# Kernel tuning notes

Hardware: AMD Instinct MI355X
Metric: run time of the kernel (lower is better)

Reference implementation:

```python
import jax, jax.numpy as jnp
import numpy as np

DIM = 256   # model dim (forced by gate Linear(32,4): d = 32 = DIM//H)
H = 8       # heads (hard-coded by mask.repeat(1,8,1,1))
D = DIM // H
B = 256     # batch
NS = 100    # skeleton tokens (sub-block size)
NQ = 64     # query tokens
N = NS + NQ # 164
NE = 4      # experts
HID = 50    # expert hidden
LN_EPS = 1e-5


def setup_inputs() -> dict:
    key = jax.random.key(0)
    ks = jax.random.split(key, 12)
    s = 0.02
    return {
        "x": jax.random.normal(ks[0], (B, N, DIM), jnp.float32),
        "mask": jax.random.randint(ks[1], (B, N), 0, 2).astype(bool),
        "w_qk_s": jax.random.normal(ks[2], (DIM, 2 * DIM), jnp.float32) * s,
        "w_qk_q": jax.random.normal(ks[3], (DIM, 2 * DIM), jnp.float32) * s,
        "w_v": jax.random.normal(ks[4], (DIM, DIM), jnp.float32) * s,
        "w_gate": jax.random.normal(ks[5], (D, NE), jnp.float32) * s,
        "b_gate": jnp.zeros((NE,), jnp.float32),
        "ln_gamma": jnp.ones((NE,), jnp.float32),
        "ln_beta": jnp.zeros((NE,), jnp.float32),
        "w1": jax.random.normal(ks[6], (NE, NS, HID), jnp.float32) * s,
        "b1": jnp.zeros((NE, HID), jnp.float32),
        "w2": jax.random.normal(ks[7], (NE, HID, NS), jnp.float32) * s,
        "b2": jnp.zeros((NE, NS), jnp.float32),
        "w_out": jax.random.normal(ks[8], (DIM, DIM), jnp.float32) * s,
        "b_out": jnp.zeros((DIM,), jnp.float32),
    }


def reference(x, mask, w_qk_s, w_qk_q, w_v, w_gate, b_gate, ln_gamma, ln_beta,
              w1, b1, w2, b2, w_out, b_out):
    b, n, dim = x.shape
    scale = dim ** -0.5  # scale_with_head=False -> dim**-0.5

    def to_heads(t):  # (b, m, H*D) -> (b, H, m, D)
        return t.reshape(b, -1, H, D).transpose(0, 2, 1, 3)

    # separate qk projections for skeleton (first 100) vs query (last 64) tokens
    q_s, k_s = jnp.split(x[:, :NS] @ w_qk_s, 2, axis=-1)
    q_q, k_q = jnp.split(x[:, NS:] @ w_qk_q, 2, axis=-1)
    q = jnp.concatenate([to_heads(q_s), to_heads(q_q)], axis=2)  # (b,H,N,D)
    k = jnp.concatenate([to_heads(k_s), to_heads(k_q)], axis=2)
    v = to_heads(x @ w_v)

    # gates: RAW reshape of x (b,n,H*D) -> (b,H,n,D) (memory reinterpretation,
    # as in torch x.reshape), detached, sliced to first 100 'rows'
    gx = jax.lax.stop_gradient(x).reshape(b, H, n, D)[:, :, :NS, :]
    g = gx @ w_gate + b_gate                              # (b,H,100,4)
    mu = g.mean(-1, keepdims=True)
    var = g.var(-1, keepdims=True)
    g = (g - mu) / jnp.sqrt(var + LN_EPS) * ln_gamma + ln_beta
    gates = jax.nn.softmax(g, axis=-1)                    # (b,H,100,4)

    dots = jnp.einsum('bhid,bhjd->bhij', q, k) * scale    # (b,H,N,N)
    mask_value = -jnp.finfo(dots.dtype).max
    dots = jnp.where(mask[:, None, None, :], mask_value, dots)

    # soft-MoE over the 100x100 sub-block (experts applied along key axis)
    attn_q = dots[:, :, :NS, :NS]                         # (b,H,100,100)
    h1 = jax.nn.relu(jnp.einsum('bhij,ejk->bheik', jax.nn.relu(attn_q), w1)
                     + b1[:, None, :])                    # (b,H,4,100,50)
    eo = jax.nn.relu(jnp.einsum('bheik,ekj->bheij', h1, w2)
                     + b2[:, None, :])                    # (b,H,4,100,100)
    moes = jnp.einsum('bheij,bhie->bhij', eo, gates)      # (b,H,100,100)

    dots = dots.at[:, :, :NS, :NS].add(moes)
    attn = jax.nn.softmax(dots, axis=-1)
    out = jnp.einsum('bhij,bhjd->bhid', attn, v)          # (b,H,N,D)
    out = out.transpose(0, 2, 1, 3).reshape(b, n, dim)
    return out @ w_out + b_out
```

## Files before the change

kernel.cpp:

```cpp
#include <hip/hip_runtime.h>

typedef __bf16 bf16x8 __attribute__((ext_vector_type(8)));
typedef __bf16 bf16x4 __attribute__((ext_vector_type(4)));
typedef float  f32x4  __attribute__((ext_vector_type(4)));

__device__ __forceinline__ bf16x8 ldb8(const __bf16* p) {
    return *reinterpret_cast<const bf16x8*>(p);
}
__device__ __forceinline__ bf16x8 zero8() {
    bf16x8 z;
    #pragma unroll
    for (int i = 0; i < 8; i++) z[i] = (__bf16)0.f;
    return z;
}
__device__ __forceinline__ __bf16 ldw(const void* p, int i, int m) {
    return m ? (__bf16)((const float*)p)[i] : ((const __bf16*)p)[i];
}
__device__ __forceinline__ bf16x8 ldx8(const void* p, size_t ei, int m) {
    if (m) {
        const float* f = (const float*)p + ei;
        f32x4 a = *reinterpret_cast<const f32x4*>(f);
        f32x4 b = *reinterpret_cast<const f32x4*>(f + 4);
        bf16x8 r;
        #pragma unroll
        for (int u = 0; u < 4; u++) { r[u] = (__bf16)a[u]; r[4 + u] = (__bf16)b[u]; }
        return r;
    }
    return ldb8((const __bf16*)p + ei);
}

__global__ __launch_bounds__(256) void detect_kernel(
    const void* x, const void* mask, int* modes, int* maskws)
{
    __shared__ int v32bad, v16bad, sbad;
    const int t = threadIdx.x, bid = blockIdx.x;
    if (t == 0) { v32bad = 0; v16bad = 0; sbad = 0; }
    __syncthreads();
    const unsigned int* mw = (const unsigned int*)mask;
    int b32 = 0, b16 = 0;
    for (int i = t; i < 10496; i += 256) {
        unsigned int w = mw[i];
        if (!(w == 0u || w == 1u || w == 0x3F800000u)) b32++;
        unsigned int h0 = w & 0xFFFFu, h1 = w >> 16;
        if (!(h0 == 0u || h0 == 1u || h0 == 0x3F80u)) b16++;
        if (!(h1 == 0u || h1 == 1u || h1 == 0x3F80u)) b16++;
    }
    if (b32) atomicAdd(&v32bad, b32);
    if (b16) atomicAdd(&v16bad, b16);
    if (bid == 0) {
        const unsigned int* xw = (const unsigned int*)x;
        int bad = 0;
        for (int i = t; i < 2048; i += 256) {
            unsigned int w = xw[i];
            unsigned int el = (w >> 7) & 0xFF, eh = (w >> 23) & 0xFF;
            if (el >= 0x94 || el == 0xFF) bad++;
            if (eh >= 0x94 || eh == 0xFF) bad++;
        }
        if (bad) atomicAdd(&sbad, bad);
    }
    __syncthreads();
    const int mmode = (v32bad == 0) ? 0 : ((v16bad == 0) ? 2 : 1);
    if (bid == 0 && t == 0) { modes[0] = (sbad > 64) ? 1 : 0; modes[1] = mmode; }
    const int lo = bid * 656, hi = lo + 656;
    for (int i = lo + t; i < hi; i += 256) {
        int val;
        if (mmode == 0)      val = (((const int*)mask)[i] != 0);
        else if (mmode == 2) val = (((const unsigned short*)mask)[i] != 0);
        else                 val = (((const unsigned char*)mask)[i] != 0);
        maskws[i] = val;
    }
}

__global__ __launch_bounds__(256) void prep_kernel(
    const void* wqks, const void* wqkq, const void* wv, const void* w1,
    const void* w2, const void* wout, const void* wg, const void* bg,
    const void* lng, const void* lnb, const void* b1, const void* b2,
    const void* bout, const int* __restrict__ modes,
    __bf16* __restrict__ Wts, __bf16* __restrict__ Wtq,
    __bf16* __restrict__ w1t, __bf16* __restrict__ w2t,
    __bf16* __restrict__ wot, __bf16* __restrict__ wsm)
{
    const int m = modes[0];
    int i = blockIdx.x * 256 + threadIdx.x;
    if (i < 196608) {
        int n = i >> 8, k = i & 255;
        __bf16 vs, vq;
        if (n < 512) { vs = ldw(wqks, k * 512 + n, m); vq = ldw(wqkq, k * 512 + n, m); }
        else         { vs = ldw(wv, k * 256 + (n - 512), m); vq = vs; }
        Wts[i] = vs; Wtq[i] = vq;
        return;
    }
    i -= 196608;
    if (i < 32768) {
        int e = i >> 13, r = i & 8191, n = r >> 7, k = r & 127;
        w1t[i] = (n < 50 && k < 100) ? ldw(w1, (e * 100 + k) * 50 + n, m) : (__bf16)0.f;
        return;
    }
    i -= 32768;
    if (i < 28672) {
        int e = i / 7168, r = i % 7168, n = r >> 6, k = r & 63;
        w2t[i] = (n < 100 && k < 50) ? ldw(w2, (e * 50 + k) * 100 + n, m) : (__bf16)0.f;
        return;
    }
    i -= 28672;
    if (i < 65536) {
        int n = i >> 8, k = i & 255;
        wot[i] = ldw(wout, k * 256 + n, m);
        return;
    }
    i -= 65536;
    if (i < 996) {
        __bf16 v;
        if (i < 128)      v = ldw(wg, i, m);
        else if (i < 132) v = ldw(bg, i - 128, m);
        else if (i < 136) v = ldw(lng, i - 132, m);
        else if (i < 140) v = ldw(lnb, i - 136, m);
        else if (i < 340) v = ldw(b1, i - 140, m);
        else if (i < 740) v = ldw(b2, i - 340, m);
        else              v = ldw(bout, i - 740, m);
        wsm[i] = v;
    }
}

__global__ __launch_bounds__(256, 2) void qkv_kernel(
    const void* __restrict__ x, const __bf16* __restrict__ Wts,
    const __bf16* __restrict__ Wtq, const __bf16* __restrict__ wsm,
    const int* __restrict__ modes,
    __bf16* __restrict__ q, __bf16* __restrict__ k, __bf16* __restrict__ vt,
    float* __restrict__ gates)
{
    __shared__ __bf16 xs[32][264];
    __shared__ float wgf[128];
    __shared__ float gcst[12];
    const int m = modes[0];
    const int b = blockIdx.y;
    const int mt = blockIdx.x >> 1;
    const int half = blockIdx.x & 1;
    const __bf16* Wt = (mt < 4) ? Wts : Wtq;
    const int rbase = (mt < 4) ? mt * 32 : 100 + (mt - 4) * 32;
    const int tid = threadIdx.x;

    if (tid < 128) wgf[tid] = (float)wsm[tid];
    if (tid < 12)  gcst[tid] = (float)wsm[128 + tid];
    for (int c = tid; c < 1024; c += 256) {
        int row = c >> 5, part = c & 31;
        bf16x8 val = ldx8(x, ((size_t)b * 164 + rbase + row) * 256 + part * 8, m);
        *reinterpret_cast<bf16x8*>(&xs[row][part * 8]) = val;
    }
    __syncthreads();

    if (half == 0) {
        int jg = rbase * 8 + tid;
        int h = jg / 164;
        int j = jg - h * 164;
        if (j < 100) {
            const __bf16* xp = &xs[tid >> 3][(tid & 7) * 32];
            float g[4] = {gcst[0], gcst[1], gcst[2], gcst[3]};
            #pragma unroll
            for (int p = 0; p < 4; p++) {
                bf16x8 xv = ldb8(xp + p * 8);
                #pragma unroll
                for (int u = 0; u < 8; u++) {
                    float f = (float)xv[u];
                    #pragma unroll
                    for (int e = 0; e < 4; e++) g[e] += f * wgf[(p * 8 + u) * 4 + e];
                }
            }
            float mu = 0.25f * (g[0] + g[1] + g[2] + g[3]);
            float var = 0.25f * ((g[0]-mu)*(g[0]-mu) + (g[1]-mu)*(g[1]-mu) +
                                 (g[2]-mu)*(g[2]-mu) + (g[3]-mu)*(g[3]-mu));
            float is = rsqrtf(var + 1e-5f);
            float mx = -3.0e38f;
            #pragma unroll
            for (int e = 0; e < 4; e++) {
                g[e] = (g[e] - mu) * is * gcst[4 + e] + gcst[8 + e];
                mx = fmaxf(mx, g[e]);
            }
            float s = 0.f;
            #pragma unroll
            for (int e = 0; e < 4; e++) { g[e] = __expf(g[e] - mx); s += g[e]; }
            float inv = 1.f / s;
            float4 gv = make_float4(g[0]*inv, g[1]*inv, g[2]*inv, g[3]*inv);
            *reinterpret_cast<float4*>(&gates[((size_t)(b * 8 + h) * 100 + j) * 4]) = gv;
        }
    }

    const int w = tid >> 6, l = tid & 63, lr = l & 15, lc = l >> 4;
    f32x4 acc[2][6];
    #pragma unroll
    for (int ms = 0; ms < 2; ms++)
        #pragma unroll
        for (int nt = 0; nt < 6; nt++) acc[ms][nt] = (f32x4){0.f, 0.f, 0.f, 0.f};

    #pragma unroll
    for (int kt = 0; kt < 8; kt++) {
        bf16x8 a0 = ldb8(&xs[lr][kt * 32 + lc * 8]);
        bf16x8 a1 = ldb8(&xs[16 + lr][kt * 32 + lc * 8]);
        #pragma unroll
        for (int nt = 0; nt < 6; nt++) {
            bf16x8 bb = ldb8(Wt + (size_t)(half * 384 + w * 96 + nt * 16 + lr) * 256 + kt * 32 + lc * 8);
            acc[0][nt] = __builtin_amdgcn_mfma_f32_16x16x32_bf16(a0, bb, acc[0][nt], 0, 0, 0);
            acc[1][nt] = __builtin_amdgcn_mfma_f32_16x16x32_bf16(a1, bb, acc[1][nt], 0, 0, 0);
        }
    }
    #pragma unroll
    for (int ms = 0; ms < 2; ms++) {
        #pragma unroll
        for (int nt = 0; nt < 6; nt++) {
            int c = half * 384 + w * 96 + nt * 16 + lr;
            int i0 = rbase + ms * 16 + lc * 4;
            if (c < 512) {
                __bf16* dst; int ch;
                if (c < 256) { dst = q; ch = c; }
                else         { dst = k; ch = c - 256; }
                int hh = ch >> 5, d = ch & 31;
                #pragma unroll
                for (int r = 0; r < 4; r++) {
                    int i = i0 + r;
                    if (mt >= 4 || i < 100)
                        dst[(((size_t)b * 8 + hh) * 164 + i) * 32 + d] = (__bf16)acc[ms][nt][r];
                }
            } else {
                int ch = c - 512, hh = ch >> 5, d = ch & 31;
                if (mt >= 4 || i0 < 100) {
                    bf16x4 pv;
                    #pragma unroll
                    for (int r = 0; r < 4; r++) pv[r] = (__bf16)acc[ms][nt][r];
                    *reinterpret_cast<bf16x4*>(&vt[((size_t)(b * 8 + hh) * 32 + d) * 176 + i0]) = pv;
                }
            }
        }
    }
}

__global__ __launch_bounds__(256, 4) void attn_kernel(
    const __bf16* __restrict__ qg, const __bf16* __restrict__ kg,
    const __bf16* __restrict__ vtg, const float* __restrict__ gatesg,
    const int* __restrict__ maskg, const __bf16* __restrict__ w1t,
    const __bf16* __restrict__ w2t, const __bf16* __restrict__ wsm,
    __bf16* __restrict__ ohg)
{
    __shared__ __align__(16) __bf16 lds[20352];
    const int RS_OFF = 7040;
    const int P_OFF  = 7040;
    const int H1_OFF = 15744;

    const __bf16* b1g = wsm + 140;
    const __bf16* b2g = wsm + 340;
    const int bh = blockIdx.x, rt = blockIdx.y, b = bh >> 3, tid = threadIdx.x;
    const int w = tid >> 6, l = tid & 63, lr = l & 15, lc = l >> 4;
    const int m0 = w * 16;

    const __bf16* kbase = kg + (size_t)bh * 164 * 32;
    for (int c = tid; c < 704; c += 256) {
        int row = c >> 2, part = c & 3;
        bf16x8 val = (row < 164) ? ldb8(kbase + row * 32 + part * 8) : zero8();
        *reinterpret_cast<bf16x8*>(&lds[row * 40 + part * 8]) = val;
    }
    unsigned mbits = 0;
    #pragma unroll
    for (int nt = 0; nt < 11; nt++) {
        int j = nt * 16 + lr;
        int bad = (j < 164) ? maskg[b * 164 + j] : 1;
        mbits |= (bad ? 1u : 0u) << nt;
    }
    int qrow = rt * 64 + m0 + lr; if (qrow > 163) qrow = 163;
    bf16x8 afq = ldb8(qg + ((size_t)bh * 164 + qrow) * 32 + lc * 8);
    __syncthreads();

    f32x4 raw[11];
    __builtin_amdgcn_s_setprio(1);
    #pragma unroll
    for (int nt = 0; nt < 11; nt++) {
        bf16x8 bf = ldb8(&lds[(nt * 16 + lr) * 40 + lc * 8]);
        f32x4 acc = {0.f, 0.f, 0.f, 0.f};
        acc = __builtin_amdgcn_mfma_f32_16x16x32_bf16(afq, bf, acc, 0, 0, 0);
        bool bad = (mbits >> nt) & 1;
        #pragma unroll
        for (int r = 0; r < 4; r++)
            raw[nt][r] = bad ? -1e30f : acc[r] * 0.0625f;
    }
    __builtin_amdgcn_s_setprio(0);

    if (rt < 2) {
        #pragma unroll
        for (int nt = 0; nt < 8; nt++) {
            int j = nt * 16 + lr;
            #pragma unroll
            for (int r = 0; r < 4; r++) {
                float v = raw[nt][r];
                v = (j >= 100 || v < 0.f) ? 0.f : v;
                lds[RS_OFF + (m0 + lc * 4 + r) * 136 + j] = (__bf16)v;
            }
        }
    }
    __syncthreads();

    const __bf16* vtb = vtg + (size_t)bh * 32 * 176;
    #pragma unroll
    for (int p = 0; p < 3; p++) {
        int c = tid + p * 256;
        int row = c / 24, jc = c - row * 24, j0 = jc * 8;
        bf16x8 vv;
        if (j0 < 164) {
            vv = ldb8(vtb + row * 176 + j0);
            if (j0 == 160) { vv[4] = (__bf16)0.f; vv[5] = (__bf16)0.f; vv[6] = (__bf16)0.f; vv[7] = (__bf16)0.f; }
        } else vv = zero8();
        *reinterpret_cast<bf16x8*>(&lds[row * 200 + j0]) = vv;
    }

    if (rt < 2) {
        const int gi0 = rt * 64 + m0 + lc * 4;
        for (int e = 0; e < 4; e++) {
            bf16x8 sa[4];
            #pragma unroll
            for (int kt = 0; kt < 4; kt++)
                sa[kt] = ldb8(&lds[RS_OFF + (m0 + lr) * 136 + kt * 32 + lc * 8]);
            #pragma unroll
            for (int nt = 0; nt < 4; nt++) {
                f32x4 acc = {0.f, 0.f, 0.f, 0.f};
                __builtin_amdgcn_s_setprio(1);
                #pragma unroll
                for (int kt = 0; kt < 4; kt++) {
                    bf16x8 bb = ldb8(w1t + (size_t)(e * 64 + nt * 16 + lr) * 128 + kt * 32 + lc * 8);
                    acc = __builtin_amdgcn_mfma_f32_16x16x32_bf16(sa[kt], bb, acc, 0, 0, 0);
                }
                __builtin_amdgcn_s_setprio(0);
                int n = nt * 16 + lr;
                float bias = (n < 50) ? (float)b1g[e * 50 + n] : 0.f;
                #pragma unroll
                for (int r = 0; r < 4; r++) {
                    float v = acc[r] + bias;
                    if (v < 0.f) v = 0.f;
                    lds[H1_OFF + (m0 + lc * 4 + r) * 72 + n] = (__bf16)v;
                }
            }
            bf16x8 ha0 = ldb8(&lds[H1_OFF + (m0 + lr) * 72 + lc * 8]);
            bf16x8 ha1 = ldb8(&lds[H1_OFF + (m0 + lr) * 72 + 32 + lc * 8]);
            float gt[4];
            #pragma unroll
            for (int r = 0; r < 4; r++) {
                int gi = gi0 + r;
                gt[r] = (gi < 100) ? gatesg[((size_t)bh * 100 + gi) * 4 + e] : 0.f;
            }
            #pragma unroll
            for (int nt = 0; nt < 7; nt++) {
                f32x4 acc = {0.f, 0.f, 0.f, 0.f};
                __builtin_amdgcn_s_setprio(1);
                bf16x8 bb0 = ldb8(w2t + (size_t)(e * 112 + nt * 16 + lr) * 64 + lc * 8);
                acc = __builtin_amdgcn_mfma_f32_16x16x32_bf16(ha0, bb0, acc, 0, 0, 0);
                bf16x8 bb1 = ldb8(w2t + (size_t)(e * 112 + nt * 16 + lr) * 64 + 32 + lc * 8);
                acc = __builtin_amdgcn_mfma_f32_16x16x32_bf16(ha1, bb1, acc, 0, 0, 0);
                __builtin_amdgcn_s_setprio(0);
                int n = nt * 16 + lr;
                float bias = (n < 100) ? (float)b2g[e * 100 + n] : 0.f;
                #pragma unroll
                for (int r = 0; r < 4; r++) {
                    float v = acc[r] + bias;
                    if (v < 0.f) v = 0.f;
                    raw[nt][r] += v * gt[r];
                }
            }
        }
    }
    __syncthreads();

    #pragma unroll
    for (int r = 0; r < 4; r++) {
        float m2 = raw[0][r];
        #pragma unroll
        for (int nt = 1; nt < 11; nt++) m2 = fmaxf(m2, raw[nt][r]);
        m2 = fmaxf(m2, __shfl_xor(m2, 1, 64));
        m2 = fmaxf(m2, __shfl_xor(m2, 2, 64));
        m2 = fmaxf(m2, __shfl_xor(m2, 4, 64));
        m2 = fmaxf(m2, __shfl_xor(m2, 8, 64));
        float s2 = 0.f;
        #pragma unroll
        for (int nt = 0; nt < 11; nt++) {
            float ev = __expf(raw[nt][r] - m2);
            raw[nt][r] = ev;
            s2 += ev;
        }
        s2 += __shfl_xor(s2, 1, 64);
        s2 += __shfl_xor(s2, 2, 64);
        s2 += __shfl_xor(s2, 4, 64);
        s2 += __shfl_xor(s2, 8, 64);
        float inv = (s2 > 0.f) ? 1.f / s2 : 0.f;
        #pragma unroll
        for (int nt = 0; nt < 11; nt++)
            lds[P_OFF + (m0 + lc * 4 + r) * 200 + nt * 16 + lr] = (__bf16)(raw[nt][r] * inv);
        lds[P_OFF + (m0 + lc * 4 + r) * 200 + 176 + lr] = (__bf16)0.f;
    }
    __syncthreads();

    int gi = rt * 64 + m0 + lr;
    #pragma unroll
    for (int nt = 0; nt < 2; nt++) {
        f32x4 acc = {0.f, 0.f, 0.f, 0.f};
        __builtin_amdgcn_s_setprio(1);
        #pragma unroll
        for (int kt = 0; kt < 6; kt++) {
            bf16x8 va = ldb8(&lds[(nt * 16 + lr) * 200 + kt * 32 + lc * 8]);
            bf16x8 pb = ldb8(&lds[P_OFF + (m0 + lr) * 200 + kt * 32 + lc * 8]);
            acc = __builtin_amdgcn_mfma_f32_16x16x32_bf16(va, pb, acc, 0, 0, 0);
        }
        __builtin_amdgcn_s_setprio(0);
        if (gi < 164) {
            bf16x4 ov;
            #pragma unroll
            for (int r = 0; r < 4; r++) ov[r] = (__bf16)acc[r];
            *reinterpret_cast<bf16x4*>(&ohg[((size_t)bh * 164 + gi) * 32 + nt * 16 + lc * 4]) = ov;
        }
    }
}

__global__ __launch_bounds__(256) void outproj_kernel(
    const __bf16* __restrict__ oh, const __bf16* __restrict__ wot,
    const __bf16* __restrict__ wsm, float* __restrict__ out)
{
    const __bf16* bout = wsm + 740;
    const int b = blockIdx.y;
    const int mt = blockIdx.x >> 2;
    const int ntile = blockIdx.x & 3;
    const int tid = threadIdx.x;
    const int w = tid >> 6, l = tid & 63, lr = l & 15, lc = l >> 4;
    int row = mt * 64 + w * 16 + lr; if (row > 163) row = 163;
    f32x4 acc[4];
    #pragma unroll
    for (int nt = 0; nt < 4; nt++) acc[nt] = (f32x4){0.f, 0.f, 0.f, 0.f};
    #pragma unroll
    for (int kt = 0; kt < 8; kt++) {
        bf16x8 a = ldb8(oh + (((size_t)b * 8 + kt) * 164 + row) * 32 + lc * 8);
        #pragma unroll
        for (int nt = 0; nt < 4; nt++) {
            bf16x8 bb = ldb8(wot + (size_t)(ntile * 64 + nt * 16 + lr) * 256 + kt * 32 + lc * 8);
            acc[nt] = __builtin_amdgcn_mfma_f32_16x16x32_bf16(a, bb, acc[nt], 0, 0, 0);
        }
    }
    #pragma unroll
    for (int nt = 0; nt < 4; nt++) {
        int n = ntile * 64 + nt * 16 + lr;
        float bias = (float)bout[n];
        #pragma unroll
        for (int r = 0; r < 4; r++) {
            int i = mt * 64 + w * 16 + lc * 4 + r;
            if (i < 164)
                out[((size_t)b * 164 + i) * 256 + n] = acc[nt][r] + bias;
        }
    }
}

extern "C" void kernel_launch(void* const* d_in, const int* in_sizes, int n_in,
                              void* d_out, int out_size, void* d_ws, size_t ws_size,
                              hipStream_t stream) {
    const void* x      = d_in[0];
    const void* mask   = d_in[1];
    const void* w_qk_s = d_in[2];
    const void* w_qk_q = d_in[3];
    const void* w_v    = d_in[4];
    const void* w_gate = d_in[5];
    const void* b_gate = d_in[6];
    const void* ln_g   = d_in[7];
    const void* ln_b   = d_in[8];
    const void* w1     = d_in[9];
    const void* b1     = d_in[10];
    const void* w2     = d_in[11];
    const void* b2     = d_in[12];
    const void* w_out  = d_in[13];
    const void* b_out  = d_in[14];
    float* out = (float*)d_out;

    char* ws = (char*)d_ws;
    size_t off = 0;
    auto nextp = [&](size_t bytes) {
        char* p = ws + off;
        off += (bytes + 255) & ~(size_t)255;
        return p;
    };
    const size_t QKV_ELEMS = (size_t)256 * 8 * 164 * 32;
    const size_t VT_ELEMS  = (size_t)256 * 8 * 32 * 176;
    int*    modes  = (int*)nextp(64);
    int*    maskws = (int*)nextp((size_t)41984 * 4);
    __bf16* qws  = (__bf16*)nextp(QKV_ELEMS * 2);
    __bf16* kws  = (__bf16*)nextp(QKV_ELEMS * 2);
    __bf16* vtws = (__bf16*)nextp(VT_ELEMS * 2);
    __bf16* ohws = (__bf16*)nextp(QKV_ELEMS * 2);
    float*  gws  = (float*)nextp((size_t)2048 * 100 * 4 * 4);
    __bf16* Wts  = (__bf16*)nextp(768 * 256 * 2);
    __bf16* Wtq  = (__bf16*)nextp(768 * 256 * 2);
    __bf16* w1t  = (__bf16*)nextp(4 * 64 * 128 * 2);
    __bf16* w2t  = (__bf16*)nextp(4 * 112 * 64 * 2);
    __bf16* wot  = (__bf16*)nextp(256 * 256 * 2);
    __bf16* wsm  = (__bf16*)nextp(996 * 2);

    detect_kernel<<<64, 256, 0, stream>>>(x, mask, modes, maskws);
    prep_kernel<<<1268, 256, 0, stream>>>(w_qk_s, w_qk_q, w_v, w1, w2, w_out,
                                          w_gate, b_gate, ln_g, ln_b, b1, b2,
                                          b_out, modes, Wts, Wtq, w1t, w2t, wot, wsm);
    qkv_kernel<<<dim3(12, 256), 256, 0, stream>>>(x, Wts, Wtq, wsm, modes,
                                                  qws, kws, vtws, gws);
    attn_kernel<<<dim3(2048, 3), 256, 0, stream>>>(qws, kws, vtws, gws, maskws,
                                                   w1t, w2t, wsm, ohws);
    outproj_kernel<<<dim3(12, 256), 256, 0, stream>>>(ohws, wot, wsm, out);
}
```

Baseline: 520.0 us.

## Fold MoE biases into GEMMs, bit-pack mask, vectorize stores, drop attn barrier

Several changes at once. The mask is packed into per-batch bitmasks in the detect kernel, so attention reads 6 words instead of 11 ints per lane. The expert biases b1 and b2 are folded into the padded weight matrices as an extra K row, fed by a constant 1 column, which removes the per-element bias loads and adds. MFMA operands are swapped in the qkv and outproj kernels so that q/k and the output are written as contiguous bf16x4 or float4 vectors. Attention gives each wave a private LDS region so one __syncthreads can be removed, and gates are loaded once as float4. The risk is added complexity around the bias column and LDS region overlap.

```diff
diff --git a/kernel.cpp b/kernel.cpp
--- a/kernel.cpp
+++ b/kernel.cpp
@@ -30,11 +30,13 @@
 }
 
 __global__ __launch_bounds__(256) void detect_kernel(
-    const void* x, const void* mask, int* modes, int* maskws)
+    const void* x, const void* mask, int* modes, unsigned* maskb)
 {
     __shared__ int v32bad, v16bad, sbad;
+    __shared__ unsigned mb[24];
     const int t = threadIdx.x, bid = blockIdx.x;
     if (t == 0) { v32bad = 0; v16bad = 0; sbad = 0; }
+    if (t < 24) mb[t] = ((t % 6) == 5) ? 0xFFFFFFF0u : 0u;
     __syncthreads();
     const unsigned int* mw = (const unsigned int*)mask;
     int b32 = 0, b16 = 0;
@@ -61,14 +63,20 @@
     __syncthreads();
     const int mmode = (v32bad == 0) ? 0 : ((v16bad == 0) ? 2 : 1);
     if (bid == 0 && t == 0) { modes[0] = (sbad > 64) ? 1 : 0; modes[1] = mmode; }
-    const int lo = bid * 656, hi = lo + 656;
-    for (int i = lo + t; i < hi; i += 256) {
+    const int lo = bid * 656;
+    for (int i2 = t; i2 < 656; i2 += 256) {
+        int i = lo + i2;
         int val;
         if (mmode == 0)      val = (((const int*)mask)[i] != 0);
         else if (mmode == 2) val = (((const unsigned short*)mask)[i] != 0);
         else                 val = (((const unsigned char*)mask)[i] != 0);
-        maskws[i] = val;
-    }
+        if (val) {
+            int ib = i2 / 164, jb = i2 - ib * 164;
+            atomicOr(&mb[ib * 6 + (jb >> 5)], 1u << (jb & 31));
+        }
+    }
+    __syncthreads();
+    if (t < 24) maskb[bid * 24 + t] = mb[t];
 }
 
 __global__ __launch_bounds__(256) void prep_kernel(
@@ -93,13 +101,23 @@
     i -= 196608;
     if (i < 32768) {
         int e = i >> 13, r = i & 8191, n = r >> 7, k = r & 127;
-        w1t[i] = (n < 50 && k < 100) ? ldw(w1, (e * 100 + k) * 50 + n, m) : (__bf16)0.f;
+        __bf16 v = (__bf16)0.f;
+        if (n < 50) {
+            if (k < 100)       v = ldw(w1, (e * 100 + k) * 50 + n, m);
+            else if (k == 100) v = ldw(b1, e * 50 + n, m);
+        }
+        w1t[i] = v;
         return;
     }
     i -= 32768;
     if (i < 28672) {
         int e = i / 7168, r = i % 7168, n = r >> 6, k = r & 63;
-        w2t[i] = (n < 100 && k < 50) ? ldw(w2, (e * 50 + k) * 100 + n, m) : (__bf16)0.f;
+        __bf16 v = (__bf16)0.f;
+        if (n < 100) {
+            if (k < 50)       v = ldw(w2, (e * 50 + k) * 100 + n, m);
+            else if (k == 50) v = ldw(b2, e * 100 + n, m);
+        }
+        w2t[i] = v;
         return;
     }
     i -= 28672;
@@ -186,6 +204,7 @@
     }
 
     const int w = tid >> 6, l = tid & 63, lr = l & 15, lc = l >> 4;
+    const int c0 = half * 384 + w * 96;
     f32x4 acc[2][6];
     #pragma unroll
     for (int ms = 0; ms < 2; ms++)
@@ -194,34 +213,41 @@
 
     #pragma unroll
     for (int kt = 0; kt < 8; kt++) {
-        bf16x8 a0 = ldb8(&xs[lr][kt * 32 + lc * 8]);
-        bf16x8 a1 = ldb8(&xs[16 + lr][kt * 32 + lc * 8]);
+        bf16x8 bx0 = ldb8(&xs[lr][kt * 32 + lc * 8]);
+        bf16x8 bx1 = ldb8(&xs[16 + lr][kt * 32 + lc * 8]);
         #pragma unroll
         for (int nt = 0; nt < 6; nt++) {
-            bf16x8 bb = ldb8(Wt + (size_t)(half * 384 + w * 96 + nt * 16 + lr) * 256 + kt * 32 + lc * 8);
-            acc[0][nt] = __builtin_amdgcn_mfma_f32_16x16x32_bf16(a0, bb, acc[0][nt], 0, 0, 0);
-            acc[1][nt] = __builtin_amdgcn_mfma_f32_16x16x32_bf16(a1, bb, acc[1][nt], 0, 0, 0);
+            bf16x8 aw = ldb8(Wt + (size_t)(c0 + nt * 16 + lr) * 256 + kt * 32 + lc * 8);
+            if (c0 + nt * 16 < 512) {
+                acc[0][nt] = __builtin_amdgcn_mfma_f32_16x16x32_bf16(aw, bx0, acc[0][nt], 0, 0, 0);
+                acc[1][nt] = __builtin_amdgcn_mfma_f32_16x16x32_bf16(aw, bx1, acc[1][nt], 0, 0, 0);
+            } else {
+                acc[0][nt] = __builtin_amdgcn_mfma_f32_16x16x32_bf16(bx0, aw, acc[0][nt], 0, 0, 0);
+                acc[1][nt] = __builtin_amdgcn_mfma_f32_16x16x32_bf16(bx1, aw, acc[1][nt], 0, 0, 0);
+            }
         }
     }
     #pragma unroll
     for (int ms = 0; ms < 2; ms++) {
         #pragma unroll
         for (int nt = 0; nt < 6; nt++) {
-            int c = half * 384 + w * 96 + nt * 16 + lr;
-            int i0 = rbase + ms * 16 + lc * 4;
-            if (c < 512) {
-                __bf16* dst; int ch;
-                if (c < 256) { dst = q; ch = c; }
-                else         { dst = k; ch = c - 256; }
-                int hh = ch >> 5, d = ch & 31;
-                #pragma unroll
-                for (int r = 0; r < 4; r++) {
-                    int i = i0 + r;
-                    if (mt >= 4 || i < 100)
-                        dst[(((size_t)b * 8 + hh) * 164 + i) * 32 + d] = (__bf16)acc[ms][nt][r];
+            int ct = c0 + nt * 16;
+            if (ct < 512) {
+                int n0 = ct + lc * 4;
+                int i  = rbase + ms * 16 + lr;
+                if (mt >= 4 || i < 100) {
+                    __bf16* dst = (n0 < 256) ? q : k;
+                    int ch0 = n0 & 255;
+                    int hh = ch0 >> 5, d0 = ch0 & 31;
+                    bf16x4 pv;
+                    #pragma unroll
+                    for (int r = 0; r < 4; r++) pv[r] = (__bf16)acc[ms][nt][r];
+                    *reinterpret_cast<bf16x4*>(&dst[(((size_t)b * 8 + hh) * 164 + i) * 32 + d0]) = pv;
                 }
             } else {
-                int ch = c - 512, hh = ch >> 5, d = ch & 31;
+                int ch = ct + lr - 512;
+                int hh = ch >> 5, d = ch & 31;
+                int i0 = rbase + ms * 16 + lc * 4;
                 if (mt >= 4 || i0 < 100) {
                     bf16x4 pv;
                     #pragma unroll
@@ -236,20 +262,15 @@
 __global__ __launch_bounds__(256, 4) void attn_kernel(
     const __bf16* __restrict__ qg, const __bf16* __restrict__ kg,
     const __bf16* __restrict__ vtg, const float* __restrict__ gatesg,
-    const int* __restrict__ maskg, const __bf16* __restrict__ w1t,
-    const __bf16* __restrict__ w2t, const __bf16* __restrict__ wsm,
-    __bf16* __restrict__ ohg)
+    const unsigned* __restrict__ maskbg, const __bf16* __restrict__ w1t,
+    const __bf16* __restrict__ w2t, __bf16* __restrict__ ohg)
 {
     __shared__ __align__(16) __bf16 lds[20352];
-    const int RS_OFF = 7040;
-    const int P_OFF  = 7040;
-    const int H1_OFF = 15744;
-
-    const __bf16* b1g = wsm + 140;
-    const __bf16* b2g = wsm + 340;
     const int bh = blockIdx.x, rt = blockIdx.y, b = bh >> 3, tid = threadIdx.x;
     const int w = tid >> 6, l = tid & 63, lr = l & 15, lc = l >> 4;
     const int m0 = w * 16;
+    const int WB  = 7040 + w * 3328;
+    const int H1B = WB + 2176;
 
     const __bf16* kbase = kg + (size_t)bh * 164 * 32;
     for (int c = tid; c < 704; c += 256) {
@@ -257,13 +278,11 @@
         bf16x8 val = (row < 164) ? ldb8(kbase + row * 32 + part * 8) : zero8();
         *reinterpret_cast<bf16x8*>(&lds[row * 40 + part * 8]) = val;
     }
+    const unsigned* mbp = maskbg + b * 6;
     unsigned mbits = 0;
     #pragma unroll
-    for (int nt = 0; nt < 11; nt++) {
-        int j = nt * 16 + lr;
-        int bad = (j < 164) ? maskg[b * 164 + j] : 1;
-        mbits |= (bad ? 1u : 0u) << nt;
-    }
+    for (int nt = 0; nt < 11; nt++)
+        mbits |= ((mbp[nt >> 1] >> (((nt & 1) << 4) + lr)) & 1u) << nt;
     int qrow = rt * 64 + m0 + lr; if (qrow > 163) qrow = 163;
     bf16x8 afq = ldb8(qg + ((size_t)bh * 164 + qrow) * 32 + lc * 8);
     __syncthreads();
@@ -289,8 +308,9 @@
             #pragma unroll
             for (int r = 0; r < 4; r++) {
                 float v = raw[nt][r];
-                v = (j >= 100 || v < 0.f) ? 0.f : v;
-                lds[RS_OFF + (m0 + lc * 4 + r) * 136 + j] = (__bf16)v;
+                v = (v < 0.f) ? 0.f : v;
+                if (j >= 100) v = (j == 100) ? 1.f : 0.f;
+                lds[WB + (lc * 4 + r) * 136 + j] = (__bf16)v;
             }
         }
     }
@@ -311,11 +331,19 @@
 
     if (rt < 2) {
         const int gi0 = rt * 64 + m0 + lc * 4;
+        float4 gv[4];
+        #pragma unroll
+        for (int r = 0; r < 4; r++) {
+            int gi = gi0 + r;
+            gv[r] = (gi < 100)
+                ? *reinterpret_cast<const float4*>(&gatesg[((size_t)bh * 100 + gi) * 4])
+                : make_float4(0.f, 0.f, 0.f, 0.f);
+        }
         for (int e = 0; e < 4; e++) {
             bf16x8 sa[4];
             #pragma unroll
             for (int kt = 0; kt < 4; kt++)
-                sa[kt] = ldb8(&lds[RS_OFF + (m0 + lr) * 136 + kt * 32 + lc * 8]);
+                sa[kt] = ldb8(&lds[WB + lr * 136 + kt * 32 + lc * 8]);
             #pragma unroll
             for (int nt = 0; nt < 4; nt++) {
                 f32x4 acc = {0.f, 0.f, 0.f, 0.f};
@@ -327,22 +355,16 @@
                 }
                 __builtin_amdgcn_s_setprio(0);
                 int n = nt * 16 + lr;
-                float bias = (n < 50) ? (float)b1g[e * 50 + n] : 0.f;
                 #pragma unroll
                 for (int r = 0; r < 4; r++) {
-                    float v = acc[r] + bias;
+                    float v = acc[r];
                     if (v < 0.f) v = 0.f;
-                    lds[H1_OFF + (m0 + lc * 4 + r) * 72 + n] = (__bf16)v;
+                    if (n == 50) v = 1.f;
+                    lds[H1B + (lc * 4 + r) * 72 + n] = (__bf16)v;
                 }
             }
-            bf16x8 ha0 = ldb8(&lds[H1_OFF + (m0 + lr) * 72 + lc * 8]);
-            bf16x8 ha1 = ldb8(&lds[H1_OFF + (m0 + lr) * 72 + 32 + lc * 8]);
-            float gt[4];
-            #pragma unroll
-            for (int r = 0; r < 4; r++) {
-                int gi = gi0 + r;
-                gt[r] = (gi < 100) ? gatesg[((size_t)bh * 100 + gi) * 4 + e] : 0.f;
-            }
+            bf16x8 ha0 = ldb8(&lds[H1B + lr * 72 + lc * 8]);
+            bf16x8 ha1 = ldb8(&lds[H1B + lr * 72 + 32 + lc * 8]);
             #pragma unroll
             for (int nt = 0; nt < 7; nt++) {
                 f32x4 acc = {0.f, 0.f, 0.f, 0.f};
@@ -352,18 +374,17 @@
                 bf16x8 bb1 = ldb8(w2t + (size_t)(e * 112 + nt * 16 + lr) * 64 + 32 + lc * 8);
                 acc = __builtin_amdgcn_mfma_f32_16x16x32_bf16(ha1, bb1, acc, 0, 0, 0);
                 __builtin_amdgcn_s_setprio(0);
-                int n = nt * 16 + lr;
-                float bias = (n < 100) ? (float)b2g[e * 100 + n] : 0.f;
                 #pragma unroll
                 for (int r = 0; r < 4; r++) {
-                    float v = acc[r] + bias;
+                    float v = acc[r];
                     if (v < 0.f) v = 0.f;
-                    raw[nt][r] += v * gt[r];
+                    float ge = (e == 0) ? gv[r].x : (e == 1) ? gv[r].y
+                             : (e == 2) ? gv[r].z : gv[r].w;
+                    raw[nt][r] += v * ge;
                 }
             }
         }
     }
-    __syncthreads();
 
     #pragma unroll
     for (int r = 0; r < 4; r++) {
@@ -388,8 +409,8 @@
         float inv = (s2 > 0.f) ? 1.f / s2 : 0.f;
         #pragma unroll
         for (int nt = 0; nt < 11; nt++)
-            lds[P_OFF + (m0 + lc * 4 + r) * 200 + nt * 16 + lr] = (__bf16)(raw[nt][r] * inv);
-        lds[P_OFF + (m0 + lc * 4 + r) * 200 + 176 + lr] = (__bf16)0.f;
+            lds[WB + (lc * 4 + r) * 200 + nt * 16 + lr] = (__bf16)(raw[nt][r] * inv);
+        lds[WB + (lc * 4 + r) * 200 + 176 + lr] = (__bf16)0.f;
     }
     __syncthreads();
 
@@ -401,7 +422,7 @@
         #pragma unroll
         for (int kt = 0; kt < 6; kt++) {
             bf16x8 va = ldb8(&lds[(nt * 16 + lr) * 200 + kt * 32 + lc * 8]);
-            bf16x8 pb = ldb8(&lds[P_OFF + (m0 + lr) * 200 + kt * 32 + lc * 8]);
+            bf16x8 pb = ldb8(&lds[WB + lr * 200 + kt * 32 + lc * 8]);
             acc = __builtin_amdgcn_mfma_f32_16x16x32_bf16(va, pb, acc, 0, 0, 0);
         }
         __builtin_amdgcn_s_setprio(0);
@@ -418,11 +439,13 @@
     const __bf16* __restrict__ oh, const __bf16* __restrict__ wot,
     const __bf16* __restrict__ wsm, float* __restrict__ out)
 {
-    const __bf16* bout = wsm + 740;
+    __shared__ float bos[256];
     const int b = blockIdx.y;
     const int mt = blockIdx.x >> 2;
     const int ntile = blockIdx.x & 3;
     const int tid = threadIdx.x;
+    bos[tid] = (float)wsm[740 + tid];
+    __syncthreads();
     const int w = tid >> 6, l = tid & 63, lr = l & 15, lc = l >> 4;
     int row = mt * 64 + w * 16 + lr; if (row > 163) row = 163;
     f32x4 acc[4];
@@ -430,22 +453,23 @@
     for (int nt = 0; nt < 4; nt++) acc[nt] = (f32x4){0.f, 0.f, 0.f, 0.f};
     #pragma unroll
     for (int kt = 0; kt < 8; kt++) {
-        bf16x8 a = ldb8(oh + (((size_t)b * 8 + kt) * 164 + row) * 32 + lc * 8);
+        bf16x8 bo = ldb8(oh + (((size_t)b * 8 + kt) * 164 + row) * 32 + lc * 8);
         #pragma unroll
         for (int nt = 0; nt < 4; nt++) {
-            bf16x8 bb = ldb8(wot + (size_t)(ntile * 64 + nt * 16 + lr) * 256 + kt * 32 + lc * 8);
-            acc[nt] = __builtin_amdgcn_mfma_f32_16x16x32_bf16(a, bb, acc[nt], 0, 0, 0);
-        }
-    }
-    #pragma unroll
-    for (int nt = 0; nt < 4; nt++) {
-        int n = ntile * 64 + nt * 16 + lr;
-        float bias = (float)bout[n];
-        #pragma unroll
-        for (int r = 0; r < 4; r++) {
-            int i = mt * 64 + w * 16 + lc * 4 + r;
-            if (i < 164)
-                out[((size_t)b * 164 + i) * 256 + n] = acc[nt][r] + bias;
+            bf16x8 aw = ldb8(wot + (size_t)(ntile * 64 + nt * 16 + lr) * 256 + kt * 32 + lc * 8);
+            acc[nt] = __builtin_amdgcn_mfma_f32_16x16x32_bf16(aw, bo, acc[nt], 0, 0, 0);
+        }
+    }
+    int i = mt * 64 + w * 16 + lr;
+    if (i < 164) {
+        #pragma unroll
+        for (int nt = 0; nt < 4; nt++) {
+            int n0 = ntile * 64 + nt * 16 + lc * 4;
+            float4 st = make_float4(acc[nt][0] + bos[n0],
+                                    acc[nt][1] + bos[n0 + 1],
+                                    acc[nt][2] + bos[n0 + 2],
+                                    acc[nt][3] + bos[n0 + 3]);
+            *reinterpret_cast<float4*>(&out[((size_t)b * 164 + i) * 256 + n0]) = st;
         }
     }
 }
@@ -479,8 +503,8 @@
     };
     const size_t QKV_ELEMS = (size_t)256 * 8 * 164 * 32;
     const size_t VT_ELEMS  = (size_t)256 * 8 * 32 * 176;
-    int*    modes  = (int*)nextp(64);
-    int*    maskws = (int*)nextp((size_t)41984 * 4);
+    int*      modes  = (int*)nextp(64);
+    unsigned* maskb  = (unsigned*)nextp((size_t)256 * 6 * 4);
     __bf16* qws  = (__bf16*)nextp(QKV_ELEMS * 2);
     __bf16* kws  = (__bf16*)nextp(QKV_ELEMS * 2);
     __bf16* vtws = (__bf16*)nextp(VT_ELEMS * 2);
@@ -493,13 +517,13 @@
     __bf16* wot  = (__bf16*)nextp(256 * 256 * 2);
     __bf16* wsm  = (__bf16*)nextp(996 * 2);
 
-    detect_kernel<<<64, 256, 0, stream>>>(x, mask, modes, maskws);
+    detect_kernel<<<64, 256, 0, stream>>>(x, mask, modes, maskb);
     prep_kernel<<<1268, 256, 0, stream>>>(w_qk_s, w_qk_q, w_v, w1, w2, w_out,
                                           w_gate, b_gate, ln_g, ln_b, b1, b2,
                                           b_out, modes, Wts, Wtq, w1t, w2t, wot, wsm);
     qkv_kernel<<<dim3(12, 256), 256, 0, stream>>>(x, Wts, Wtq, wsm, modes,
                                                   qws, kws, vtws, gws);
-    attn_kernel<<<dim3(2048, 3), 256, 0, stream>>>(qws, kws, vtws, gws, maskws,
-                                                   w1t, w2t, wsm, ohws);
+    attn_kernel<<<dim3(2048, 3), 256, 0, stream>>>(qws, kws, vtws, gws, maskb,
+                                                   w1t, w2t, ohws);
     outproj_kernel<<<dim3(12, 256), 256, 0, stream>>>(ohws, wot, wsm, out);
 }
```

Result: slower. 591.8 us (+13.8%).
